# Kernel optimization log

Measured on AMD Instinct MI355X. Metric: run time of the kernel, lower is better.

## Reference

```python
import jax, jax.numpy as jnp
import numpy as np

T, B, IN_DIM, H = 4096, 2048, 1, 10  # len(input), seq_length, input_dim, hidden_dim


def setup_inputs() -> dict:
    key = jax.random.key(0)
    ks = jax.random.split(key, 11)
    s_in = 1.0 / np.sqrt(H)  # torch LSTM/Linear init scale
    u = lambda k, shape: jax.random.uniform(k, shape, jnp.float32, -s_in, s_in)
    return {
        "x": jax.random.normal(ks[0], (T, B, IN_DIM), jnp.float32),
        # layer 0 (input_size=1), layer 1 (input_size=H); torch gate order i,f,g,o
        "W_ih0": u(ks[1], (4 * H, IN_DIM)),
        "W_hh0": u(ks[2], (4 * H, H)),
        "b_ih0": u(ks[3], (4 * H,)),
        "b_hh0": u(ks[4], (4 * H,)),
        "W_ih1": u(ks[5], (4 * H, H)),
        "W_hh1": u(ks[6], (4 * H, H)),
        "b_ih1": u(ks[7], (4 * H,)),
        "b_hh1": u(ks[8], (4 * H,)),
        "W_lin": u(ks[9], (1, H)),
        "b_lin": u(ks[10], (1,)),
    }


def _lstm_layer(x, W_ih, W_hh, b_ih, b_hh):
    # x: (T, B, in); precompute input contributions for all timesteps at once
    xw = jnp.einsum("tbi,gi->tbg", x, W_ih) + b_ih + b_hh  # (T, B, 4H)
    Whh_T = W_hh.T

    def step(carry, xt):
        h, c = carry
        gates = xt + h @ Whh_T  # (B, 4H)
        i, f, g, o = jnp.split(gates, 4, axis=-1)
        i = jax.nn.sigmoid(i)
        f = jax.nn.sigmoid(f)
        g = jnp.tanh(g)
        o = jax.nn.sigmoid(o)
        c = f * c + i * g
        h = o * jnp.tanh(c)
        return (h, c), h

    b = x.shape[1]
    h0 = jnp.zeros((b, W_hh.shape[1]), x.dtype)
    _, hs = jax.lax.scan(step, (h0, h0), xw)
    return hs  # (T, B, H)


def reference(x, W_ih0, W_hh0, b_ih0, b_hh0, W_ih1, W_hh1, b_ih1, b_hh1, W_lin, b_lin):
    h1 = _lstm_layer(x, W_ih0, W_hh0, b_ih0, b_hh0)   # (T, B, H)
    h2 = _lstm_layer(h1, W_ih1, W_hh1, b_ih1, b_hh1)  # (T, B, H)
    # faithful to original: view(seq_length, len(input), H)[-1] is a raw reshape
    last = h2.reshape(B, T, H)[-1]                    # (T, H)
    return last @ W_lin.T + b_lin                     # (T, 1)
```

## Files before the change

kernel.cpp:

```cpp
#include <hip/hip_runtime.h>

namespace {

constexpr int T_STEPS = 4096;
constexpr int NBATCH  = 2048;
constexpr int HID     = 10;
constexpr float L2E   = 1.4426950408889634f;

typedef float v2f __attribute__((ext_vector_type(2)));
typedef float v4f __attribute__((ext_vector_type(4)));

__device__ __forceinline__ float ex2(float x){ return __builtin_amdgcn_exp2f(x); }
__device__ __forceinline__ float rcp_(float x){ return __builtin_amdgcn_rcpf(x); }

template<int IMM>
__device__ __forceinline__ float swz(float v){
    return __int_as_float(__builtin_amdgcn_ds_swizzle(__float_as_int(v), IMM));
}
__device__ __forceinline__ float bperm(int addr, float v){
    return __int_as_float(__builtin_amdgcn_ds_bpermute(addr, __float_as_int(v)));
}
template<int CTRL>
__device__ __forceinline__ float dpp(float v){
    return __int_as_float(__builtin_amdgcn_update_dpp(0, __float_as_int(v), CTRL, 0xF, 0xF, true));
}
__device__ __forceinline__ void pk_fma(v2f &a, v2f b, v2f c){
    asm("v_pk_fma_f32 %0, %1, %2, %0" : "+v"(a) : "v"(b), "v"(c));
}
__device__ __forceinline__ float rdlane(float v, int lane){
    return __int_as_float(__builtin_amdgcn_readlane(__float_as_int(v), lane));
}


template<bool OUT>
__device__ __forceinline__ void lstm_step(
    const v2f (&Wp)[2][5], float wx0, float wx1, float b0, float b1,
    float selA, float kA, float kB,
    float* hwp, const char* rdb,
    v4f &Va, v4f &Vb, v2f &Vc,
    float &hn, float &c, float xv,
    float wlin, float blin, int t_l1, float* out, int b)
{
    const v2f va01 = __builtin_shufflevector(Va, Va, 0, 1);
    const v2f va23 = __builtin_shufflevector(Va, Va, 2, 3);
    const v2f vb01 = __builtin_shufflevector(Vb, Vb, 0, 1);
    const v2f vb23 = __builtin_shufflevector(Vb, Vb, 2, 3);
    const v2f vc01 = Vc;

    v2f A0 = { fmaf(wx0, xv, b0), 0.0f };
    v2f A1 = { fmaf(wx1, xv, b1), 0.0f };
    pk_fma(A0, Wp[0][0], va01);  pk_fma(A1, Wp[1][0], va01);
    pk_fma(A0, Wp[0][1], va23);  pk_fma(A1, Wp[1][1], va23);
    pk_fma(A0, Wp[0][2], vb01);  pk_fma(A1, Wp[1][2], vb01);
    pk_fma(A0, Wp[0][3], vb23);  pk_fma(A1, Wp[1][3], vb23);
    pk_fma(A0, Wp[0][4], vc01);  pk_fma(A1, Wp[1][4], vc01);
    float a0 = A0.x + A0.y;
    float a1 = A1.x + A1.y;

    a0 = fmaf(selA, dpp<0x108>(a0), a0);
    a1 = fmaf(selA, dpp<0x108>(a1), a1);

    const float e0 = ex2(a0), e1 = ex2(a1);
    const float d0 = 1.0f + e0, d1 = 1.0f + e1;
    const float rD = rcp_(d0 * d1);
    const float r0 = d1 * rD;
    const float r1 = d0 * rD;
    const float g0 = fmaf(kA, r0, kB);
    const float g1 = r1;

    const float gv = dpp<0x101>(g0);
    const float ov = dpp<0x101>(g1);
    c = fmaf(g1, c, g0 * gv);
    const float tc = fmaf(-2.0f, rcp_(1.0f + ex2(c * (2.0f*L2E))), 1.0f);
    hn = ov * tc;

    *hwp = hn;
    asm volatile("" ::: "memory");
    Va = *(const v4f*)(rdb);
    Vb = *(const v4f*)(rdb+16);
    Vc = *(const v2f*)(rdb+32);

    if (OUT) {
        float p = hn * wlin;
        p += swz<0x041F>(p); p += swz<0x081F>(p); p += swz<0x101F>(p);
        p += swz<0x201F>(p); p += swz<0x401F>(p);
        p += bperm((((int)threadIdx.x ^ 32) & 63)*4, p);
        if (threadIdx.x == 0)
            out[(t_l1 - (T_STEPS-2))*NBATCH + b] = p + blin;
    }
}

__global__ __launch_bounds__(64) void lstm2_kernel(
    const float* __restrict__ x,
    const float* __restrict__ Wih0, const float* __restrict__ Whh0,
    const float* __restrict__ bih0, const float* __restrict__ bhh0,
    const float* __restrict__ Wih1, const float* __restrict__ Whh1,
    const float* __restrict__ bih1, const float* __restrict__ bhh1,
    const float* __restrict__ Wlin, const float* __restrict__ blin_p,
    float* __restrict__ out)
{
    __shared__ __attribute__((aligned(16))) float hx[112];

    const int tid = (int)threadIdx.x;
    const int b   = (int)blockIdx.x;

    int role, q;
    if      (tid < 16){ role=0; q=tid; }
    else if (tid < 24){ role=1; q=tid-16; }
    else if (tid < 32){ role=2; q=tid-24; }
    else if (tid < 40){ role=1; q=tid-32+8; }
    else if (tid < 48){ role=2; q=tid-40+8; }
    else if (tid < 52){ role=1; q=tid-48+16; }
    else if (tid < 56){ role=0; q=tid-52+16; }
    else if (tid < 60){ role=2; q=tid-56+16; }
    else              { role=3; q=0; }
    const int h = q >> 1, p = q & 1;
    const int gate0 = p ? 2 : 0, gate1 = p ? 3 : 1;
    const float s0 = (gate0 == 2) ? 2.0f*L2E : -L2E;
    const float s1 = -L2E;

    float W0[HID], W1[HID], wx0=0.0f, wx1=0.0f, b0=0.0f, b1=0.0f;
    const int r0i = gate0*HID + h, r1i = gate1*HID + h;
    if (role == 0){
        #pragma unroll
        for (int j=0;j<HID;++j){ W0[j]=Whh0[r0i*HID+j]*s0; W1[j]=Whh0[r1i*HID+j]*s1; }
        wx0 = Wih0[r0i]*s0;  wx1 = Wih0[r1i]*s1;
        b0 = (bih0[r0i]+bhh0[r0i])*s0;  b1 = (bih0[r1i]+bhh0[r1i])*s1;
    } else if (role == 1){
        #pragma unroll
        for (int j=0;j<HID;++j){ W0[j]=Wih1[r0i*HID+j]*s0; W1[j]=Wih1[r1i*HID+j]*s1; }
        b0 = (bih1[r0i]+bhh1[r0i])*s0;  b1 = (bih1[r1i]+bhh1[r1i])*s1;
    } else if (role == 2){
        #pragma unroll
        for (int j=0;j<HID;++j){ W0[j]=Whh1[r0i*HID+j]*s0; W1[j]=Whh1[r1i*HID+j]*s1; }
    } else {
        #pragma unroll
        for (int j=0;j<HID;++j){ W0[j]=0.0f; W1[j]=0.0f; }
    }
    v2f Wp[2][5];
    #pragma unroll
    for (int k=0;k<5;++k){ Wp[0][k]=v2f{W0[2*k],W0[2*k+1]}; Wp[1][k]=v2f{W1[2*k],W1[2*k+1]}; }

    const float selA = (role==1) ? 1.0f : 0.0f;
    const float kA = p ? -2.0f : 1.0f;
    const float kB = p ?  1.0f : 0.0f;
    const bool owner = (p==0) && (role==0 || role==1);
    const int wslot = owner ? (role==0 ? h : 12+h) : (48+tid);
    float* hwp = &hx[wslot];
    const char* rdb = (const char*)hx + (role==2 ? 48 : 0);
    const float wlin = (role==1 && p==0) ? Wlin[h] : 0.0f;
    const float blin = blin_p[0];

    float hn = 0.0f, c = 0.0f;
    v4f Va = {0,0,0,0}, Vb = {0,0,0,0};
    v2f Vc = {0,0};

    const float* xp = x + (size_t)(tid & 7) * NBATCH + b;
    float xcur = xp[0];
    float xnxt = xp[(size_t)8 * NBATCH];

    {
        const float zb0 = (role==0) ? b0 : 0.0f, zb1 = (role==0) ? b1 : 0.0f;
        lstm_step<false>(Wp, wx0,wx1, zb0,zb1, selA,kA,kB, hwp,rdb, Va,Vb,Vc, hn,c, rdlane(xcur,0), wlin,blin, 0, out, b);
        lstm_step<false>(Wp, wx0,wx1, b0,b1, selA,kA,kB, hwp,rdb, Va,Vb,Vc, hn,c, rdlane(xcur,1), wlin,blin, 0, out, b);
        lstm_step<false>(Wp, wx0,wx1, b0,b1, selA,kA,kB, hwp,rdb, Va,Vb,Vc, hn,c, rdlane(xcur,2), wlin,blin, 0, out, b);
        lstm_step<false>(Wp, wx0,wx1, b0,b1, selA,kA,kB, hwp,rdb, Va,Vb,Vc, hn,c, rdlane(xcur,3), wlin,blin, 0, out, b);
        lstm_step<false>(Wp, wx0,wx1, b0,b1, selA,kA,kB, hwp,rdb, Va,Vb,Vc, hn,c, rdlane(xcur,4), wlin,blin, 0, out, b);
        lstm_step<false>(Wp, wx0,wx1, b0,b1, selA,kA,kB, hwp,rdb, Va,Vb,Vc, hn,c, rdlane(xcur,5), wlin,blin, 0, out, b);
        lstm_step<false>(Wp, wx0,wx1, b0,b1, selA,kA,kB, hwp,rdb, Va,Vb,Vc, hn,c, rdlane(xcur,6), wlin,blin, 0, out, b);
        lstm_step<false>(Wp, wx0,wx1, b0,b1, selA,kA,kB, hwp,rdb, Va,Vb,Vc, hn,c, rdlane(xcur,7), wlin,blin, 0, out, b);
    }

    for (int i=1; i<511; ++i){
        xcur = xnxt;
        xnxt = xp[(size_t)(i+1)*8*NBATCH];
        lstm_step<false>(Wp, wx0,wx1, b0,b1, selA,kA,kB, hwp,rdb, Va,Vb,Vc, hn,c, rdlane(xcur,0), wlin,blin, 0, out, b);
        lstm_step<false>(Wp, wx0,wx1, b0,b1, selA,kA,kB, hwp,rdb, Va,Vb,Vc, hn,c, rdlane(xcur,1), wlin,blin, 0, out, b);
        lstm_step<false>(Wp, wx0,wx1, b0,b1, selA,kA,kB, hwp,rdb, Va,Vb,Vc, hn,c, rdlane(xcur,2), wlin,blin, 0, out, b);
        lstm_step<false>(Wp, wx0,wx1, b0,b1, selA,kA,kB, hwp,rdb, Va,Vb,Vc, hn,c, rdlane(xcur,3), wlin,blin, 0, out, b);
        lstm_step<false>(Wp, wx0,wx1, b0,b1, selA,kA,kB, hwp,rdb, Va,Vb,Vc, hn,c, rdlane(xcur,4), wlin,blin, 0, out, b);
        lstm_step<false>(Wp, wx0,wx1, b0,b1, selA,kA,kB, hwp,rdb, Va,Vb,Vc, hn,c, rdlane(xcur,5), wlin,blin, 0, out, b);
        lstm_step<false>(Wp, wx0,wx1, b0,b1, selA,kA,kB, hwp,rdb, Va,Vb,Vc, hn,c, rdlane(xcur,6), wlin,blin, 0, out, b);
        lstm_step<false>(Wp, wx0,wx1, b0,b1, selA,kA,kB, hwp,rdb, Va,Vb,Vc, hn,c, rdlane(xcur,7), wlin,blin, 0, out, b);
    }

    {
        xcur = xnxt;
        lstm_step<false>(Wp, wx0,wx1, b0,b1, selA,kA,kB, hwp,rdb, Va,Vb,Vc, hn,c, rdlane(xcur,0), wlin,blin, 0, out, b);
        lstm_step<false>(Wp, wx0,wx1, b0,b1, selA,kA,kB, hwp,rdb, Va,Vb,Vc, hn,c, rdlane(xcur,1), wlin,blin, 0, out, b);
        lstm_step<false>(Wp, wx0,wx1, b0,b1, selA,kA,kB, hwp,rdb, Va,Vb,Vc, hn,c, rdlane(xcur,2), wlin,blin, 0, out, b);
        lstm_step<false>(Wp, wx0,wx1, b0,b1, selA,kA,kB, hwp,rdb, Va,Vb,Vc, hn,c, rdlane(xcur,3), wlin,blin, 0, out, b);
        lstm_step<false>(Wp, wx0,wx1, b0,b1, selA,kA,kB, hwp,rdb, Va,Vb,Vc, hn,c, rdlane(xcur,4), wlin,blin, 0, out, b);
        lstm_step<false>(Wp, wx0,wx1, b0,b1, selA,kA,kB, hwp,rdb, Va,Vb,Vc, hn,c, rdlane(xcur,5), wlin,blin, 0, out, b);
        lstm_step<false>(Wp, wx0,wx1, b0,b1, selA,kA,kB, hwp,rdb, Va,Vb,Vc, hn,c, rdlane(xcur,6), wlin,blin, 0, out, b);
        lstm_step<true >(Wp, wx0,wx1, b0,b1, selA,kA,kB, hwp,rdb, Va,Vb,Vc, hn,c, rdlane(xcur,7), wlin,blin, T_STEPS-2, out, b);
    }

    lstm_step<true>(Wp, wx0,wx1, b0,b1, selA,kA,kB, hwp,rdb, Va,Vb,Vc, hn,c, 0.0f, wlin,blin, T_STEPS-1, out, b);
}

}

extern "C" void kernel_launch(void* const* d_in, const int* in_sizes, int n_in,
                              void* d_out, int out_size, void* d_ws, size_t ws_size,
                              hipStream_t stream) {
    const float* x    = (const float*)d_in[0];
    const float* Wih0 = (const float*)d_in[1];
    const float* Whh0 = (const float*)d_in[2];
    const float* bih0 = (const float*)d_in[3];
    const float* bhh0 = (const float*)d_in[4];
    const float* Wih1 = (const float*)d_in[5];
    const float* Whh1 = (const float*)d_in[6];
    const float* bih1 = (const float*)d_in[7];
    const float* bhh1 = (const float*)d_in[8];
    const float* Wlin = (const float*)d_in[9];
    const float* blin = (const float*)d_in[10];
    float* out = (float*)d_out;

    hipLaunchKernelGGL(lstm2_kernel, dim3(NBATCH), dim3(64), 0, stream,
                       x, Wih0, Whh0, bih0, bhh0, Wih1, Whh1, bih1, bhh1, Wlin, blin, out);
}
```

Baseline: 829.5 us.

## Interleave two batch columns per wavefront to hide recurrence latency

Each 64-thread block now processes two independent batch elements, with their LSTM step chains interleaved. The goal is to hide the serial latency of each step (LDS round trip, DPP, transcendental ops) by overlapping two independent dependency chains, and to halve the grid to 1024 blocks. The shared combined reciprocal for the two sigmoids is replaced by two separate reciprocals, which shortens the dependency chain but issues more transcendental instructions. The costs are higher register pressure, more LDS use, and fewer wavefronts available to fill the CUs.

Measured after the change: 986.2 us. 18.9% more time.

```diff
diff --git a/kernel.cpp b/kernel.cpp
--- a/kernel.cpp
+++ b/kernel.cpp
@@ -33,7 +33,7 @@
 
 
 template<bool OUT>
-__device__ __forceinline__ void lstm_step(
+__device__ __forceinline__ void body(
     const v2f (&Wp)[2][5], float wx0, float wx1, float b0, float b1,
     float selA, float kA, float kB,
     float* hwp, const char* rdb,
@@ -60,11 +60,8 @@
     a0 = fmaf(selA, dpp<0x108>(a0), a0);
     a1 = fmaf(selA, dpp<0x108>(a1), a1);
 
-    const float e0 = ex2(a0), e1 = ex2(a1);
-    const float d0 = 1.0f + e0, d1 = 1.0f + e1;
-    const float rD = rcp_(d0 * d1);
-    const float r0 = d1 * rD;
-    const float r1 = d0 * rD;
+    const float r0 = rcp_(1.0f + ex2(a0));
+    const float r1 = rcp_(1.0f + ex2(a1));
     const float g0 = fmaf(kA, r0, kB);
     const float g1 = r1;
 
@@ -99,10 +96,11 @@
     const float* __restrict__ Wlin, const float* __restrict__ blin_p,
     float* __restrict__ out)
 {
-    __shared__ __attribute__((aligned(16))) float hx[112];
+    __shared__ __attribute__((aligned(16))) float hx[192];
 
     const int tid = (int)threadIdx.x;
-    const int b   = (int)blockIdx.x;
+    const int bA  = 2*(int)blockIdx.x;
+    const int bB  = bA + 1;
 
     int role, q;
     if      (tid < 16){ role=0; q=tid; }
@@ -145,58 +143,71 @@
     const float kA = p ? -2.0f : 1.0f;
     const float kB = p ?  1.0f : 0.0f;
     const bool owner = (p==0) && (role==0 || role==1);
-    const int wslot = owner ? (role==0 ? h : 12+h) : (48+tid);
-    float* hwp = &hx[wslot];
-    const char* rdb = (const char*)hx + (role==2 ? 48 : 0);
+    const int slot  = owner ? (role==0 ? h : 12+h) : -1;
+    float* hwpA = &hx[slot >= 0 ? slot      : 64+tid];
+    float* hwpB = &hx[slot >= 0 ? 32+slot   : 64+tid];
+    const char* rdbA = (const char*)hx       + (role==2 ? 48 : 0);
+    const char* rdbB = (const char*)hx + 128 + (role==2 ? 48 : 0);
     const float wlin = (role==1 && p==0) ? Wlin[h] : 0.0f;
     const float blin = blin_p[0];
 
-    float hn = 0.0f, c = 0.0f;
-    v4f Va = {0,0,0,0}, Vb = {0,0,0,0};
-    v2f Vc = {0,0};
-
-    const float* xp = x + (size_t)(tid & 7) * NBATCH + b;
+    float hnA=0.0f, cA=0.0f, hnB=0.0f, cB=0.0f;
+    v4f VaA={0,0,0,0}, VbA={0,0,0,0}; v2f VcA={0,0};
+    v4f VaB={0,0,0,0}, VbB={0,0,0,0}; v2f VcB={0,0};
+
+    const int tl = tid & 15;
+    const float* xp = x + (size_t)(tl & 7) * NBATCH + ((tl >= 8) ? bB : bA);
     float xcur = xp[0];
     float xnxt = xp[(size_t)8 * NBATCH];
 
+    #define STEP2(OUTF, BS0, BS1, J, TL1)                                                   \
+        body<OUTF>(Wp, wx0,wx1, BS0,BS1, selA,kA,kB, hwpA,rdbA, VaA,VbA,VcA, hnA,cA,        \
+                   rdlane(xcur,(J)), wlin,blin, TL1, out, bA);                              \
+        body<OUTF>(Wp, wx0,wx1, BS0,BS1, selA,kA,kB, hwpB,rdbB, VaB,VbB,VcB, hnB,cB,        \
+                   rdlane(xcur,8+(J)), wlin,blin, TL1, out, bB);
+
     {
         const float zb0 = (role==0) ? b0 : 0.0f, zb1 = (role==0) ? b1 : 0.0f;
-        lstm_step<false>(Wp, wx0,wx1, zb0,zb1, selA,kA,kB, hwp,rdb, Va,Vb,Vc, hn,c, rdlane(xcur,0), wlin,blin, 0, out, b);
-        lstm_step<false>(Wp, wx0,wx1, b0,b1, selA,kA,kB, hwp,rdb, Va,Vb,Vc, hn,c, rdlane(xcur,1), wlin,blin, 0, out, b);
-        lstm_step<false>(Wp, wx0,wx1, b0,b1, selA,kA,kB, hwp,rdb, Va,Vb,Vc, hn,c, rdlane(xcur,2), wlin,blin, 0, out, b);
-        lstm_step<false>(Wp, wx0,wx1, b0,b1, selA,kA,kB, hwp,rdb, Va,Vb,Vc, hn,c, rdlane(xcur,3), wlin,blin, 0, out, b);
-        lstm_step<false>(Wp, wx0,wx1, b0,b1, selA,kA,kB, hwp,rdb, Va,Vb,Vc, hn,c, rdlane(xcur,4), wlin,blin, 0, out, b);
-        lstm_step<false>(Wp, wx0,wx1, b0,b1, selA,kA,kB, hwp,rdb, Va,Vb,Vc, hn,c, rdlane(xcur,5), wlin,blin, 0, out, b);
-        lstm_step<false>(Wp, wx0,wx1, b0,b1, selA,kA,kB, hwp,rdb, Va,Vb,Vc, hn,c, rdlane(xcur,6), wlin,blin, 0, out, b);
-        lstm_step<false>(Wp, wx0,wx1, b0,b1, selA,kA,kB, hwp,rdb, Va,Vb,Vc, hn,c, rdlane(xcur,7), wlin,blin, 0, out, b);
+        STEP2(false, zb0, zb1, 0, 0)
+        STEP2(false, b0, b1, 1, 0)
+        STEP2(false, b0, b1, 2, 0)
+        STEP2(false, b0, b1, 3, 0)
+        STEP2(false, b0, b1, 4, 0)
+        STEP2(false, b0, b1, 5, 0)
+        STEP2(false, b0, b1, 6, 0)
+        STEP2(false, b0, b1, 7, 0)
     }
 
     for (int i=1; i<511; ++i){
         xcur = xnxt;
         xnxt = xp[(size_t)(i+1)*8*NBATCH];
-        lstm_step<false>(Wp, wx0,wx1, b0,b1, selA,kA,kB, hwp,rdb, Va,Vb,Vc, hn,c, rdlane(xcur,0), wlin,blin, 0, out, b);
-        lstm_step<false>(Wp, wx0,wx1, b0,b1, selA,kA,kB, hwp,rdb, Va,Vb,Vc, hn,c, rdlane(xcur,1), wlin,blin, 0, out, b);
-        lstm_step<false>(Wp, wx0,wx1, b0,b1, selA,kA,kB, hwp,rdb, Va,Vb,Vc, hn,c, rdlane(xcur,2), wlin,blin, 0, out, b);
-        lstm_step<false>(Wp, wx0,wx1, b0,b1, selA,kA,kB, hwp,rdb, Va,Vb,Vc, hn,c, rdlane(xcur,3), wlin,blin, 0, out, b);
-        lstm_step<false>(Wp, wx0,wx1, b0,b1, selA,kA,kB, hwp,rdb, Va,Vb,Vc, hn,c, rdlane(xcur,4), wlin,blin, 0, out, b);
-        lstm_step<false>(Wp, wx0,wx1, b0,b1, selA,kA,kB, hwp,rdb, Va,Vb,Vc, hn,c, rdlane(xcur,5), wlin,blin, 0, out, b);
-        lstm_step<false>(Wp, wx0,wx1, b0,b1, selA,kA,kB, hwp,rdb, Va,Vb,Vc, hn,c, rdlane(xcur,6), wlin,blin, 0, out, b);
-        lstm_step<false>(Wp, wx0,wx1, b0,b1, selA,kA,kB, hwp,rdb, Va,Vb,Vc, hn,c, rdlane(xcur,7), wlin,blin, 0, out, b);
+        STEP2(false, b0, b1, 0, 0)
+        STEP2(false, b0, b1, 1, 0)
+        STEP2(false, b0, b1, 2, 0)
+        STEP2(false, b0, b1, 3, 0)
+        STEP2(false, b0, b1, 4, 0)
+        STEP2(false, b0, b1, 5, 0)
+        STEP2(false, b0, b1, 6, 0)
+        STEP2(false, b0, b1, 7, 0)
     }
 
     {
         xcur = xnxt;
-        lstm_step<false>(Wp, wx0,wx1, b0,b1, selA,kA,kB, hwp,rdb, Va,Vb,Vc, hn,c, rdlane(xcur,0), wlin,blin, 0, out, b);
-        lstm_step<false>(Wp, wx0,wx1, b0,b1, selA,kA,kB, hwp,rdb, Va,Vb,Vc, hn,c, rdlane(xcur,1), wlin,blin, 0, out, b);
-        lstm_step<false>(Wp, wx0,wx1, b0,b1, selA,kA,kB, hwp,rdb, Va,Vb,Vc, hn,c, rdlane(xcur,2), wlin,blin, 0, out, b);
-        lstm_step<false>(Wp, wx0,wx1, b0,b1, selA,kA,kB, hwp,rdb, Va,Vb,Vc, hn,c, rdlane(xcur,3), wlin,blin, 0, out, b);
-        lstm_step<false>(Wp, wx0,wx1, b0,b1, selA,kA,kB, hwp,rdb, Va,Vb,Vc, hn,c, rdlane(xcur,4), wlin,blin, 0, out, b);
-        lstm_step<false>(Wp, wx0,wx1, b0,b1, selA,kA,kB, hwp,rdb, Va,Vb,Vc, hn,c, rdlane(xcur,5), wlin,blin, 0, out, b);
-        lstm_step<false>(Wp, wx0,wx1, b0,b1, selA,kA,kB, hwp,rdb, Va,Vb,Vc, hn,c, rdlane(xcur,6), wlin,blin, 0, out, b);
-        lstm_step<true >(Wp, wx0,wx1, b0,b1, selA,kA,kB, hwp,rdb, Va,Vb,Vc, hn,c, rdlane(xcur,7), wlin,blin, T_STEPS-2, out, b);
-    }
-
-    lstm_step<true>(Wp, wx0,wx1, b0,b1, selA,kA,kB, hwp,rdb, Va,Vb,Vc, hn,c, 0.0f, wlin,blin, T_STEPS-1, out, b);
+        STEP2(false, b0, b1, 0, 0)
+        STEP2(false, b0, b1, 1, 0)
+        STEP2(false, b0, b1, 2, 0)
+        STEP2(false, b0, b1, 3, 0)
+        STEP2(false, b0, b1, 4, 0)
+        STEP2(false, b0, b1, 5, 0)
+        STEP2(false, b0, b1, 6, 0)
+        STEP2(true , b0, b1, 7, T_STEPS-2)
+    }
+
+    body<true>(Wp, wx0,wx1, b0,b1, selA,kA,kB, hwpA,rdbA, VaA,VbA,VcA, hnA,cA,
+               0.0f, wlin,blin, T_STEPS-1, out, bA);
+    body<true>(Wp, wx0,wx1, b0,b1, selA,kA,kB, hwpB,rdbB, VaB,VbB,VcB, hnB,cB,
+               0.0f, wlin,blin, T_STEPS-1, out, bB);
+    #undef STEP2
 }
 
 }
@@ -217,6 +228,6 @@
     const float* blin = (const float*)d_in[10];
     float* out = (float*)d_out;
 
-    hipLaunchKernelGGL(lstm2_kernel, dim3(NBATCH), dim3(64), 0, stream,
+    hipLaunchKernelGGL(lstm2_kernel, dim3(NBATCH/2), dim3(64), 0, stream,
                        x, Wih0, Whh0, bih0, bhh0, Wih1, Whh1, bih1, bhh1, Wlin, blin, out);
 }
```
